# Kernel tuning notes

Measured on AMD Instinct MI355X. Metric: run time of the kernel, lower is better.

The kernel has to match this reference:

```python
import jax, jax.numpy as jnp
import numpy as np

D_MODEL = 2048
NUM_HEADS = 16
HEAD_DIM = D_MODEL // NUM_HEADS
EPS = 1e-6


def setup_inputs() -> dict:
    key = jax.random.key(0)
    ks = jax.random.split(key, 5)
    B, S = 1, 4096
    scale = 1.0 / np.sqrt(D_MODEL)
    return {
        "x": jax.random.normal(ks[0], (B, S, D_MODEL), dtype=jnp.float32),
        "wq": jax.random.normal(ks[1], (D_MODEL, D_MODEL), dtype=jnp.float32) * scale,
        "wk": jax.random.normal(ks[2], (D_MODEL, D_MODEL), dtype=jnp.float32) * scale,
        "wv": jax.random.normal(ks[3], (D_MODEL, D_MODEL), dtype=jnp.float32) * scale,
        "wo": jax.random.normal(ks[4], (D_MODEL, D_MODEL), dtype=jnp.float32) * scale,
        "q_norm_w": jnp.ones((HEAD_DIM,), dtype=jnp.float32),
        "k_norm_w": jnp.ones((HEAD_DIM,), dtype=jnp.float32),
    }


def _rmsnorm(x, w):
    rms = jnp.sqrt(jnp.mean(x * x, axis=-1, keepdims=True) + EPS)
    return x / rms * w


def reference(x, wq, wk, wv, wo, q_norm_w, k_norm_w):
    B, S, _ = x.shape
    # nn.Linear: y = x @ W.T ; split heads -> [B, H, S, Dh]
    def proj(w):
        return (x @ w.T).reshape(B, S, NUM_HEADS, HEAD_DIM).transpose(0, 2, 1, 3)
    q = _rmsnorm(proj(wq), q_norm_w)
    k = _rmsnorm(proj(wk), k_norm_w)
    v = proj(wv)
    scale = 1.0 / np.sqrt(HEAD_DIM)
    attn = jnp.einsum("bhqd,bhkd->bhqk", q, k) * scale  # [B,H,S,S]
    attn = jax.nn.softmax(attn, axis=-1)
    out = jnp.einsum("bhqk,bhkd->bhqd", attn, v)
    out = out.transpose(0, 2, 1, 3).reshape(B, S, D_MODEL)
    return out @ wo.T
```

## Files before the change

kernel.cpp:

```cpp
#include <hip/hip_runtime.h>
#include <hip/hip_bf16.h>

#define S 4096
#define D 2048
#define NH 16
#define HD 128

typedef __attribute__((ext_vector_type(8))) short bf16x8;
typedef __attribute__((ext_vector_type(4))) float f32x4;

typedef __attribute__((address_space(1))) char glob_char;
typedef __attribute__((address_space(3))) char lds_char_t;

__device__ __forceinline__ void gld16(const void* g, void* l) {
    __builtin_amdgcn_global_load_lds((const glob_char*)g, (lds_char_t*)l, 16, 0, 0);
}

__device__ __forceinline__ unsigned short f2b(float f) {
    union { float f; unsigned u; } c; c.f = f;
    unsigned r = c.u + 0x7fff + ((c.u >> 16) & 1);
    return (unsigned short)(r >> 16);
}
__device__ __forceinline__ float b2f(unsigned short u) {
    union { unsigned u; float f; } c; c.u = ((unsigned)u) << 16;
    return c.f;
}

__global__ __launch_bounds__(256) void cvt_all(
    const float* __restrict__ x,  const float* __restrict__ wq,
    const float* __restrict__ wk, const float* __restrict__ wv,
    const float* __restrict__ wo,
    unsigned short* __restrict__ xb, unsigned short* __restrict__ wqkvb,
    unsigned short* __restrict__ wob)
{
    const int z = blockIdx.y;
    const float* src; unsigned short* dst; int n4;
    if (z == 0)      { src = x;  dst = xb;                        n4 = (S * D) / 4; }
    else if (z == 1) { src = wq; dst = wqkvb;                     n4 = (D * D) / 4; }
    else if (z == 2) { src = wk; dst = wqkvb + (size_t)D * D;     n4 = (D * D) / 4; }
    else if (z == 3) { src = wv; dst = wqkvb + 2 * (size_t)D * D; n4 = (D * D) / 4; }
    else             { src = wo; dst = wob;                       n4 = (D * D) / 4; }
    int i = blockIdx.x * 256 + threadIdx.x;
    if (i < n4) {
        float4 v = ((const float4*)src)[i];
        ushort4 o;
        o.x = f2b(v.x); o.y = f2b(v.y); o.z = f2b(v.z); o.w = f2b(v.w);
        ((ushort4*)dst)[i] = o;
    }
}

template<int OUTMODE>
__global__ __launch_bounds__(256) void gemm_nt(
    const unsigned short* __restrict__ A, const unsigned short* __restrict__ B,
    void* __restrict__ O0, void* __restrict__ O1, void* __restrict__ O2,
    const float* __restrict__ qw, const float* __restrict__ kw)
{
    __shared__ short As[128 * 32];
    __shared__ short Bs[128 * 32];
    __shared__ float red[2][128];

    const int tid = threadIdx.x;
    const int m0 = blockIdx.y * 128, n0 = blockIdx.x * 128;
    const int w = tid >> 6, lane = tid & 63, col = lane & 15, quad = lane >> 4;
    const int mw = (w >> 1) * 64, nw = (w & 1) * 64;

    const int r0 = tid >> 2, k80 = (tid & 3) << 3;
    const size_t aoff = (size_t)(m0 + r0) * 2048 + k80;
    const size_t boff = (size_t)(n0 + r0) * 2048 + k80;

    f32x4 acc[4][4];
    #pragma unroll
    for (int i = 0; i < 4; ++i)
        #pragma unroll
        for (int j = 0; j < 4; ++j)
            #pragma unroll
            for (int r = 0; r < 4; ++r) acc[i][j][r] = 0.0f;

    for (int k0 = 0; k0 < 2048; k0 += 32) {
        gld16(&A[aoff + k0],               &As[tid * 8]);
        gld16(&A[aoff + 64 * 2048 + k0],   &As[(tid + 256) * 8]);
        gld16(&B[boff + k0],               &Bs[tid * 8]);
        gld16(&B[boff + 64 * 2048 + k0],   &Bs[(tid + 256) * 8]);
        __syncthreads();
        bf16x8 af[4], bf[4];
        #pragma unroll
        for (int i = 0; i < 4; ++i)
            af[i] = *(const bf16x8*)&As[(mw + 16 * i + col) * 32 + quad * 8];
        #pragma unroll
        for (int j = 0; j < 4; ++j)
            bf[j] = *(const bf16x8*)&Bs[(nw + 16 * j + col) * 32 + quad * 8];
        #pragma unroll
        for (int i = 0; i < 4; ++i)
            #pragma unroll
            for (int j = 0; j < 4; ++j)
                acc[i][j] = __builtin_amdgcn_mfma_f32_16x16x32_bf16(af[i], bf[j], acc[i][j], 0, 0, 0);
        __syncthreads();
    }

    if (OUTMODE == 1) {
        float* C = (float*)O0;
        #pragma unroll
        for (int i = 0; i < 4; ++i)
            #pragma unroll
            for (int j = 0; j < 4; ++j)
                #pragma unroll
                for (int r = 0; r < 4; ++r)
                    C[(size_t)(m0 + mw + 16 * i + quad * 4 + r) * 2048 + n0 + nw + 16 * j + col] = acc[i][j][r];
    } else {
        const int sel = n0 >> 11;
        if (sel == 2) {
            unsigned short* VtO = (unsigned short*)O2;
            #pragma unroll
            for (int i = 0; i < 4; ++i)
                #pragma unroll
                for (int j = 0; j < 4; ++j) {
                    int n = (n0 & 2047) + nw + 16 * j + col;
                    int hh = n >> 7, dv = n & 127;
                    ushort4 pk;
                    pk.x = f2b(acc[i][j][0]); pk.y = f2b(acc[i][j][1]);
                    pk.z = f2b(acc[i][j][2]); pk.w = f2b(acc[i][j][3]);
                    *(ushort4*)&VtO[(size_t)hh * (HD * S) + (size_t)dv * S +
                                    m0 + mw + 16 * i + quad * 4] = pk;
                }
        } else {
            unsigned short* C = (unsigned short*)(sel == 0 ? O0 : O1);
            const int nc0 = (n0 & 2047) + nw + col;
            const float* wgt = (sel == 0) ? qw : kw;
            const float extra = (sel == 0) ? 0.08838834764831845f : 1.0f;
            float wv[4];
            #pragma unroll
            for (int j = 0; j < 4; ++j) wv[j] = wgt[nw + 16 * j + col];
            float rsc[4][4];
            #pragma unroll
            for (int i = 0; i < 4; ++i)
                #pragma unroll
                for (int r = 0; r < 4; ++r) {
                    float ss = 0.0f;
                    #pragma unroll
                    for (int j = 0; j < 4; ++j) ss += acc[i][j][r] * acc[i][j][r];
                    #pragma unroll
                    for (int d = 1; d < 16; d <<= 1) ss += __shfl_xor(ss, d, 64);
                    if (col == 0) red[w & 1][mw + 16 * i + quad * 4 + r] = ss;
                }
            __syncthreads();
            #pragma unroll
            for (int i = 0; i < 4; ++i)
                #pragma unroll
                for (int r = 0; r < 4; ++r) {
                    float tot = red[0][mw + 16 * i + quad * 4 + r] + red[1][mw + 16 * i + quad * 4 + r];
                    rsc[i][r] = rsqrtf(tot * (1.0f / HD) + 1e-6f) * extra;
                }
            #pragma unroll
            for (int i = 0; i < 4; ++i)
                #pragma unroll
                for (int j = 0; j < 4; ++j)
                    #pragma unroll
                    for (int r = 0; r < 4; ++r)
                        C[(size_t)(m0 + mw + 16 * i + quad * 4 + r) * 2048 + nc0 + 16 * j] =
                            f2b(acc[i][j][r] * rsc[i][r] * wv[j]);
        }
    }
}

__global__ __launch_bounds__(256, 2) void flash_mfma(
    const unsigned short* __restrict__ Qg, const unsigned short* __restrict__ Kg,
    const unsigned short* __restrict__ Vt, unsigned short* __restrict__ Ctx)
{
    __shared__ short Ks[2][4 * 64 * 32];
    __shared__ short Vs[2][2 * 128 * 32];
    __shared__ short Ps[128 * 64];

    const int tid = threadIdx.x;
    const int w = tid >> 6, lane = tid & 63, col = lane & 15, quad = lane >> 4;
    const int q0 = blockIdx.x * 128, h = blockIdx.y;
    const size_t vbase = (size_t)h * (HD * S);

    bf16x8 aq[2][4];
    #pragma unroll
    for (int qs = 0; qs < 2; ++qs) {
        const size_t qoff = (size_t)(q0 + w * 32 + qs * 16 + col) * 2048 + h * 128 + quad * 8;
        #pragma unroll
        for (int ds = 0; ds < 4; ++ds)
            aq[qs][ds] = *(const bf16x8*)&Qg[qoff + ds * 32];
    }

    float l_r[2][4] = {{0.f,0.f,0.f,0.f},{0.f,0.f,0.f,0.f}};
    f32x4 o[2][8];
    #pragma unroll
    for (int qs = 0; qs < 2; ++qs)
        #pragma unroll
        for (int nj = 0; nj < 8; ++nj)
            #pragma unroll
            for (int r = 0; r < 4; ++r) o[qs][nj][r] = 0.0f;

    auto stage = [&](int j0s, int b) {
        #pragma unroll
        for (int it = 0; it < 4; ++it) {
            int c = tid + (it << 8);
            int ds = c >> 8, rem = c & 255, key = rem >> 2, ch = rem & 3;
            int g = ch ^ ((key >> 1) & 3);
            gld16(&Kg[(size_t)(j0s + key) * 2048 + h * 128 + ds * 32 + g * 8], &Ks[b][c * 8]);
        }
        #pragma unroll
        for (int it = 0; it < 4; ++it) {
            int c = tid + (it << 8);
            int ks = c >> 9, rem = c & 511, dv = rem >> 2, ch = rem & 3;
            int g = ch ^ ((dv >> 1) & 3);
            gld16(&Vt[vbase + (size_t)dv * S + j0s + ks * 32 + g * 8], &Vs[b][c * 8]);
        }
    };

    auto compute = [&](int b) {
        f32x4 sc[2][4];
        #pragma unroll
        for (int qs = 0; qs < 2; ++qs)
            #pragma unroll
            for (int kj = 0; kj < 4; ++kj)
                #pragma unroll
                for (int r = 0; r < 4; ++r) sc[qs][kj][r] = 0.0f;
        __builtin_amdgcn_s_setprio(1);
        #pragma unroll
        for (int ds = 0; ds < 4; ++ds)
            #pragma unroll
            for (int kj = 0; kj < 4; ++kj) {
                int key = kj * 16 + col;
                bf16x8 bk = *(const bf16x8*)&Ks[b][(ds * 64 + key) * 32 +
                                                  ((quad ^ ((key >> 1) & 3)) << 3)];
                sc[0][kj] = __builtin_amdgcn_mfma_f32_16x16x32_bf16(aq[0][ds], bk, sc[0][kj], 0, 0, 0);
                sc[1][kj] = __builtin_amdgcn_mfma_f32_16x16x32_bf16(aq[1][ds], bk, sc[1][kj], 0, 0, 0);
            }
        __builtin_amdgcn_s_setprio(0);

        #pragma unroll
        for (int qs = 0; qs < 2; ++qs)
            #pragma unroll
            for (int kj = 0; kj < 4; ++kj)
                #pragma unroll
                for (int r = 0; r < 4; ++r) {
                    unsigned short pb = f2b(__expf(sc[qs][kj][r]));
                    int ql = w * 32 + qs * 16 + quad * 4 + r;
                    int kk = kj * 16 + col;
                    Ps[ql * 64 + (kk ^ ((ql & 7) << 3))] = (short)pb;
                    l_r[qs][r] += b2f(pb);
                }

        __builtin_amdgcn_s_setprio(1);
        #pragma unroll
        for (int ks = 0; ks < 2; ++ks) {
            bf16x8 ap[2];
            #pragma unroll
            for (int qs = 0; qs < 2; ++qs) {
                int qrow = w * 32 + qs * 16 + col;
                int k0 = ks * 32 + quad * 8;
                ap[qs] = *(const bf16x8*)&Ps[qrow * 64 + (k0 ^ ((qrow & 7) << 3))];
            }
            #pragma unroll
            for (int nj = 0; nj < 8; ++nj) {
                int dv = nj * 16 + col;
                bf16x8 bv = *(const bf16x8*)&Vs[b][(ks * 128 + dv) * 32 +
                                                  ((quad ^ ((dv >> 1) & 3)) << 3)];
                o[0][nj] = __builtin_amdgcn_mfma_f32_16x16x32_bf16(ap[0], bv, o[0][nj], 0, 0, 0);
                o[1][nj] = __builtin_amdgcn_mfma_f32_16x16x32_bf16(ap[1], bv, o[1][nj], 0, 0, 0);
            }
        }
        __builtin_amdgcn_s_setprio(0);
    };

    stage(0, 0);
    for (int j0 = 0; j0 < S; j0 += 128) {
        __syncthreads();
        stage(j0 + 64, 1);
        compute(0);
        __syncthreads();
        if (j0 + 128 < S) stage(j0 + 128, 0);
        compute(1);
    }

    #pragma unroll
    for (int d = 1; d < 16; d <<= 1)
        #pragma unroll
        for (int qs = 0; qs < 2; ++qs)
            #pragma unroll
            for (int r = 0; r < 4; ++r) l_r[qs][r] += __shfl_xor(l_r[qs][r], d, 64);

    #pragma unroll
    for (int qs = 0; qs < 2; ++qs) {
        float inv[4];
        #pragma unroll
        for (int r = 0; r < 4; ++r) inv[r] = 1.0f / l_r[qs][r];
        #pragma unroll
        for (int nj = 0; nj < 8; ++nj)
            #pragma unroll
            for (int r = 0; r < 4; ++r)
                Ctx[(size_t)(q0 + w * 32 + qs * 16 + quad * 4 + r) * 2048 + h * 128 + nj * 16 + col] =
                    f2b(o[qs][nj][r] * inv[r]);
    }
}

extern "C" void kernel_launch(void* const* d_in, const int* in_sizes, int n_in,
                              void* d_out, int out_size, void* d_ws, size_t ws_size,
                              hipStream_t stream)
{
    const float* x  = (const float*)d_in[0];
    const float* wq = (const float*)d_in[1];
    const float* wk = (const float*)d_in[2];
    const float* wv = (const float*)d_in[3];
    const float* wo = (const float*)d_in[4];
    const float* qw = (const float*)d_in[5];
    const float* kw = (const float*)d_in[6];
    float* out = (float*)d_out;

    const size_t MB = 1u << 20;
    char* ws = (char*)d_ws;
    unsigned short* xb    = (unsigned short*)(ws);
    unsigned short* Wqkvb = (unsigned short*)(ws + 16 * MB);
    unsigned short* Wob   = (unsigned short*)(ws + 40 * MB);
    unsigned short* Qb    = (unsigned short*)(ws + 48 * MB);
    unsigned short* Kb    = (unsigned short*)(ws + 64 * MB);
    unsigned short* Vt    = (unsigned short*)(ws + 80 * MB);
    unsigned short* Ctx   = xb;

    cvt_all<<<dim3(8192, 5), dim3(256), 0, stream>>>(x, wq, wk, wv, wo, xb, Wqkvb, Wob);

    gemm_nt<0><<<dim3(48, 32), dim3(256), 0, stream>>>(xb, Wqkvb, Qb, Kb, Vt, qw, kw);

    flash_mfma<<<dim3(32, 16), dim3(256), 0, stream>>>(Qb, Kb, Vt, Ctx);

    gemm_nt<1><<<dim3(16, 32), dim3(256), 0, stream>>>(Ctx, Wob, out, out, out, qw, kw);
}
```

Baseline: 492.2 us.

## Use exp2 with log2e folded into Q scale and compute row sums via MFMA

Folds log2(e) into the Q pre-scale so the softmax exponent becomes a native exp2, removing a multiply per score. Row sums of P are now accumulated by an extra MFMA against a vector of ones instead of per-element bf16 round-trips and a final shuffle reduction. LDS and global addresses are precomputed and pointer-incremented to cut integer ALU work in the inner loop. It adds two MFMAs per k-step and relies on the same no-max softmax assumption as before.

```diff
diff --git a/kernel.cpp b/kernel.cpp
--- a/kernel.cpp
+++ b/kernel.cpp
@@ -21,9 +21,13 @@
     unsigned r = c.u + 0x7fff + ((c.u >> 16) & 1);
     return (unsigned short)(r >> 16);
 }
-__device__ __forceinline__ float b2f(unsigned short u) {
-    union { unsigned u; float f; } c; c.u = ((unsigned)u) << 16;
-    return c.f;
+
+__device__ __forceinline__ float fexp2(float x) {
+#if __has_builtin(__builtin_amdgcn_exp2f)
+    return __builtin_amdgcn_exp2f(x);
+#else
+    return __expf(x * 0.6931471805599453f);
+#endif
 }
 
 __global__ __launch_bounds__(256) void cvt_all(
@@ -126,7 +130,8 @@
             unsigned short* C = (unsigned short*)(sel == 0 ? O0 : O1);
             const int nc0 = (n0 & 2047) + nw + col;
             const float* wgt = (sel == 0) ? qw : kw;
-            const float extra = (sel == 0) ? 0.08838834764831845f : 1.0f;
+            const float extra = (sel == 0)
+                ? 0.08838834764831845f * 1.4426950408889634f : 1.0f;
             float wv[4];
             #pragma unroll
             for (int j = 0; j < 4; ++j) wv[j] = wgt[nw + 16 * j + col];
@@ -162,18 +167,21 @@
     }
 }
 
+struct FlashSmem {
+    short Ks[2][8192];
+    short Vs[2][8192];
+    short Ps[8192];
+};
+
 __global__ __launch_bounds__(256, 2) void flash_mfma(
     const unsigned short* __restrict__ Qg, const unsigned short* __restrict__ Kg,
     const unsigned short* __restrict__ Vt, unsigned short* __restrict__ Ctx)
 {
-    __shared__ short Ks[2][4 * 64 * 32];
-    __shared__ short Vs[2][2 * 128 * 32];
-    __shared__ short Ps[128 * 64];
+    __shared__ FlashSmem sm;
 
     const int tid = threadIdx.x;
     const int w = tid >> 6, lane = tid & 63, col = lane & 15, quad = lane >> 4;
     const int q0 = blockIdx.x * 128, h = blockIdx.y;
-    const size_t vbase = (size_t)h * (HD * S);
 
     bf16x8 aq[2][4];
     #pragma unroll
@@ -184,29 +192,66 @@
             aq[qs][ds] = *(const bf16x8*)&Qg[qoff + ds * 32];
     }
 
-    float l_r[2][4] = {{0.f,0.f,0.f,0.f},{0.f,0.f,0.f,0.f}};
+    const unsigned short* kga[4];
+    const unsigned short* vga[4];
+    #pragma unroll
+    for (int it = 0; it < 4; ++it) {
+        int c = tid + (it << 8);
+        {   int ds = c >> 8, rem = c & 255, key = rem >> 2, ch = rem & 3;
+            int g = ch ^ ((key >> 1) & 3);
+            kga[it] = &Kg[(size_t)key * 2048 + h * 128 + ds * 32 + g * 8]; }
+        {   int ks = c >> 9, rem = c & 511, dv = rem >> 2, ch = rem & 3;
+            int g = ch ^ ((dv >> 1) & 3);
+            vga[it] = &Vt[(size_t)h * (HD * S) + (size_t)dv * S + ks * 32 + g * 8]; }
+    }
+
+    const int fb = col * 32 + ((quad ^ ((col >> 1) & 3)) << 3);
+    int ap_off[2][2];
+    #pragma unroll
+    for (int qs = 0; qs < 2; ++qs) {
+        int qrow = w * 32 + qs * 16 + col;
+        #pragma unroll
+        for (int ks = 0; ks < 2; ++ks) {
+            int k0 = ks * 32 + quad * 8;
+            ap_off[ks][qs] = qrow * 64 + (k0 ^ ((qrow & 7) << 3));
+        }
+    }
+    int psb2[2][4];
+    #pragma unroll
+    for (int qs = 0; qs < 2; ++qs)
+        #pragma unroll
+        for (int r = 0; r < 4; ++r) {
+            int ql = w * 32 + qs * 16 + quad * 4 + r;
+            int s = (ql & 7) << 3;
+            psb2[qs][r] = ql * 64 + (col ^ (s & 8)) + (s & 48);
+        }
+
+    bf16x8 vone;
+    #pragma unroll
+    for (int i = 0; i < 8; ++i) vone[i] = (short)0x3F80;
+
+    f32x4 lacc[2];
     f32x4 o[2][8];
     #pragma unroll
-    for (int qs = 0; qs < 2; ++qs)
+    for (int qs = 0; qs < 2; ++qs) {
+        #pragma unroll
+        for (int r = 0; r < 4; ++r) lacc[qs][r] = 0.0f;
         #pragma unroll
         for (int nj = 0; nj < 8; ++nj)
             #pragma unroll
             for (int r = 0; r < 4; ++r) o[qs][nj][r] = 0.0f;
-
-    auto stage = [&](int j0s, int b) {
+    }
+
+    auto stage = [&](int b) {
         #pragma unroll
         for (int it = 0; it < 4; ++it) {
-            int c = tid + (it << 8);
-            int ds = c >> 8, rem = c & 255, key = rem >> 2, ch = rem & 3;
-            int g = ch ^ ((key >> 1) & 3);
-            gld16(&Kg[(size_t)(j0s + key) * 2048 + h * 128 + ds * 32 + g * 8], &Ks[b][c * 8]);
+            gld16(kga[it], &sm.Ks[b][(tid + (it << 8)) * 8]);
+            kga[it] += 64 * 2048;
         }
         #pragma unroll
         for (int it = 0; it < 4; ++it) {
-            int c = tid + (it << 8);
-            int ks = c >> 9, rem = c & 511, dv = rem >> 2, ch = rem & 3;
-            int g = ch ^ ((dv >> 1) & 3);
-            gld16(&Vt[vbase + (size_t)dv * S + j0s + ks * 32 + g * 8], &Vs[b][c * 8]);
+            gld16(vga[it], &sm.Vs[b][(tid + (it << 8)) * 8]);
+            vga[it] += 64;
         }
     };
 
@@ -223,9 +268,7 @@
         for (int ds = 0; ds < 4; ++ds)
             #pragma unroll
             for (int kj = 0; kj < 4; ++kj) {
-                int key = kj * 16 + col;
-                bf16x8 bk = *(const bf16x8*)&Ks[b][(ds * 64 + key) * 32 +
-                                                  ((quad ^ ((key >> 1) & 3)) << 3)];
+                bf16x8 bk = *(const bf16x8*)&sm.Ks[b][fb + ds * 2048 + kj * 512];
                 sc[0][kj] = __builtin_amdgcn_mfma_f32_16x16x32_bf16(aq[0][ds], bk, sc[0][kj], 0, 0, 0);
                 sc[1][kj] = __builtin_amdgcn_mfma_f32_16x16x32_bf16(aq[1][ds], bk, sc[1][kj], 0, 0, 0);
             }
@@ -236,58 +279,41 @@
             #pragma unroll
             for (int kj = 0; kj < 4; ++kj)
                 #pragma unroll
-                for (int r = 0; r < 4; ++r) {
-                    unsigned short pb = f2b(__expf(sc[qs][kj][r]));
-                    int ql = w * 32 + qs * 16 + quad * 4 + r;
-                    int kk = kj * 16 + col;
-                    Ps[ql * 64 + (kk ^ ((ql & 7) << 3))] = (short)pb;
-                    l_r[qs][r] += b2f(pb);
-                }
+                for (int r = 0; r < 4; ++r)
+                    sm.Ps[psb2[qs][r] ^ (kj * 16)] = (short)f2b(fexp2(sc[qs][kj][r]));
 
         __builtin_amdgcn_s_setprio(1);
         #pragma unroll
         for (int ks = 0; ks < 2; ++ks) {
-            bf16x8 ap[2];
-            #pragma unroll
-            for (int qs = 0; qs < 2; ++qs) {
-                int qrow = w * 32 + qs * 16 + col;
-                int k0 = ks * 32 + quad * 8;
-                ap[qs] = *(const bf16x8*)&Ps[qrow * 64 + (k0 ^ ((qrow & 7) << 3))];
-            }
+            bf16x8 ap0 = *(const bf16x8*)&sm.Ps[ap_off[ks][0]];
+            bf16x8 ap1 = *(const bf16x8*)&sm.Ps[ap_off[ks][1]];
+            lacc[0] = __builtin_amdgcn_mfma_f32_16x16x32_bf16(ap0, vone, lacc[0], 0, 0, 0);
+            lacc[1] = __builtin_amdgcn_mfma_f32_16x16x32_bf16(ap1, vone, lacc[1], 0, 0, 0);
             #pragma unroll
             for (int nj = 0; nj < 8; ++nj) {
-                int dv = nj * 16 + col;
-                bf16x8 bv = *(const bf16x8*)&Vs[b][(ks * 128 + dv) * 32 +
-                                                  ((quad ^ ((dv >> 1) & 3)) << 3)];
-                o[0][nj] = __builtin_amdgcn_mfma_f32_16x16x32_bf16(ap[0], bv, o[0][nj], 0, 0, 0);
-                o[1][nj] = __builtin_amdgcn_mfma_f32_16x16x32_bf16(ap[1], bv, o[1][nj], 0, 0, 0);
+                bf16x8 bv = *(const bf16x8*)&sm.Vs[b][fb + ks * 4096 + nj * 512];
+                o[0][nj] = __builtin_amdgcn_mfma_f32_16x16x32_bf16(ap0, bv, o[0][nj], 0, 0, 0);
+                o[1][nj] = __builtin_amdgcn_mfma_f32_16x16x32_bf16(ap1, bv, o[1][nj], 0, 0, 0);
             }
         }
         __builtin_amdgcn_s_setprio(0);
     };
 
-    stage(0, 0);
+    stage(0);
     for (int j0 = 0; j0 < S; j0 += 128) {
         __syncthreads();
-        stage(j0 + 64, 1);
+        stage(1);
         compute(0);
         __syncthreads();
-        if (j0 + 128 < S) stage(j0 + 128, 0);
+        if (j0 + 128 < S) stage(0);
         compute(1);
     }
-
-    #pragma unroll
-    for (int d = 1; d < 16; d <<= 1)
-        #pragma unroll
-        for (int qs = 0; qs < 2; ++qs)
-            #pragma unroll
-            for (int r = 0; r < 4; ++r) l_r[qs][r] += __shfl_xor(l_r[qs][r], d, 64);
 
     #pragma unroll
     for (int qs = 0; qs < 2; ++qs) {
         float inv[4];
         #pragma unroll
-        for (int r = 0; r < 4; ++r) inv[r] = 1.0f / l_r[qs][r];
+        for (int r = 0; r < 4; ++r) inv[r] = 1.0f / lacc[qs][r];
         #pragma unroll
         for (int nj = 0; nj < 8; ++nj)
             #pragma unroll
```

New measurement: 472.5 us. -4.0%, faster.
